# Performance work log

Measured on AMD Instinct MI355X. Metric: run time of the kernel, lower is better.

The kernel has to match this reference:

```python
import jax, jax.numpy as jnp
import numpy as np
from jax import lax

B, C, OUT, H, W = 8, 512, 512, 64, 64
BN_EPS = 1e-5


def setup_inputs() -> dict:
    key = jax.random.key(0)
    ks = jax.random.split(key, 20)
    s = 1.0 / np.sqrt(C)
    d = {
        "input1": jax.random.normal(ks[0], (B, C, H, W), jnp.float32),
        "input2": jax.random.normal(ks[1], (B, C, H, W), jnp.float32),
        "wq1": jax.random.normal(ks[2], (C, C), jnp.float32) * s,
        "bq1": jnp.zeros((C,), jnp.float32),
        "wk1": jax.random.normal(ks[3], (C, C), jnp.float32) * s,
        "bk1": jnp.zeros((C,), jnp.float32),
        "wv1": jax.random.normal(ks[4], (C, C), jnp.float32) * s,
        "bv1": jnp.zeros((C,), jnp.float32),
        "wq2": jax.random.normal(ks[5], (C, C), jnp.float32) * s,
        "bq2": jnp.zeros((C,), jnp.float32),
        "wk2": jax.random.normal(ks[6], (C, C), jnp.float32) * s,
        "bk2": jnp.zeros((C,), jnp.float32),
        "wv2": jax.random.normal(ks[7], (C, C), jnp.float32) * s,
        "bv2": jnp.zeros((C,), jnp.float32),
        "w_lin": jax.random.normal(ks[8], (1, C), jnp.float32) * s,  # shared gate conv, no bias
        "w_cat": jax.random.normal(ks[9], (OUT, 2 * C, 3, 3), jnp.float32) * (1.0 / np.sqrt(2 * C * 9)),
        "bn_gamma": jnp.ones((OUT,), jnp.float32),
        "bn_beta": jnp.zeros((OUT,), jnp.float32),
    }
    return d


def _conv1x1(x, w, b):
    # x: [B,C,H,W], w: [O,C] -> [B,O,H,W]
    return jnp.einsum('bchw,oc->bohw', x, w) + b[None, :, None, None]


def _branch(x_q_src, x_kv_src, wq, bq, wk, bk, wv, bv, w_lin, x_resid):
    # matches: attn = softmax(k(x_kv) @ q(x_q)^T); out = attn^T @ v(x_kv)
    b, c, h, w = x_kv_src.shape
    n = h * w
    q = _conv1x1(x_q_src, wq, bq).reshape(b, c, n)      # [B,C,N] (from the OTHER input)
    k = _conv1x1(x_kv_src, wk, bk).reshape(b, c, n)
    v = _conv1x1(x_kv_src, wv, bv).reshape(b, c, n)
    attn = jnp.einsum('bkn,bcn->bkc', k, q)             # [B,C,C]
    attn = jax.nn.softmax(attn, axis=-1)
    out = jnp.einsum('bkc,bkn->bcn', attn, v).reshape(b, c, h, w)
    # sigmoid gate: linear(avgpool(x_resid)) -> scalar per batch
    pooled = jnp.mean(x_resid, axis=(2, 3))             # [B,C]
    a = jax.nn.sigmoid(pooled @ w_lin.T)                # [B,1]
    return out * a[:, :, None, None] + x_resid


def reference(input1, input2, wq1, bq1, wk1, bk1, wv1, bv1,
              wq2, bq2, wk2, bk2, wv2, bv2, w_lin, w_cat, bn_gamma, bn_beta):
    # branch 1: k1 from input1, q2 from input2, v1 from input1, gate from input1
    out1 = _branch(input2, input1, wq2, bq2, wk1, bk1, wv1, bv1, w_lin, input1)
    # branch 2: k2 from input2, q1 from input1, v2 from input2, gate from input2
    out2 = _branch(input1, input2, wq1, bq1, wk2, bk2, wv2, bv2, w_lin, input2)
    x = jnp.concatenate([out1, out2], axis=1)           # [B,2C,H,W]
    y = lax.conv_general_dilated(x, w_cat, (1, 1), 'SAME',
                                 dimension_numbers=('NCHW', 'OIHW', 'NCHW'))
    # BatchNorm2d in training mode: batch statistics over (N,H,W)
    mean = jnp.mean(y, axis=(0, 2, 3), keepdims=True)
    var = jnp.var(y, axis=(0, 2, 3), keepdims=True)
    y = (y - mean) * lax.rsqrt(var + BN_EPS)
    y = y * bn_gamma[None, :, None, None] + bn_beta[None, :, None, None]
    return jax.nn.relu(y)
```

## Files before the change

### kernel.cpp

```cpp
#include <hip/hip_runtime.h>


typedef unsigned short u16;
typedef unsigned int u32;
typedef float f32x4 __attribute__((ext_vector_type(4)));
typedef short bf16x8 __attribute__((ext_vector_type(8)));

#define DEV __device__ __forceinline__

DEV u16 f2bf(float f) {
  u32 u = __float_as_uint(f);
  return (u16)((u + 0x7fffu + ((u >> 16) & 1u)) >> 16);
}
DEV float bf2f(u16 u) { return __uint_as_float(((u32)u) << 16); }

DEV void gload_lds16(const void* g, void* l) {
  __builtin_amdgcn_global_load_lds(
      (const __attribute__((address_space(1))) void*)g,
      (__attribute__((address_space(3))) void*)l, 16, 0, 0);
}

DEV void stage_tile(u16* L, const u16* src, int row0, long ld, int k0, int wid, int lane) {
  int rr = lane >> 2;
  int cc = (lane & 3) << 3;
#pragma unroll
  for (int j = 0; j < 2; ++j) {
    int chunk = j * 4 + wid;
    const u16* g = src + (long)(row0 + chunk * 16 + rr) * ld + (k0 + cc);
    gload_lds16(g, L + chunk * 512);
  }
}

DEV float waveRedSum(float v) {
#pragma unroll
  for (int o = 32; o > 0; o >>= 1) v += __shfl_xor(v, o);
  return v;
}

DEV float blockReduceSum256(float v) {
  __shared__ float r[4];
  v = waveRedSum(v);
  int tid = threadIdx.x;
  if ((tid & 63) == 0) r[tid >> 6] = v;
  __syncthreads();
  return r[0] + r[1] + r[2] + r[3];
}

__global__ __launch_bounds__(256) void gemm_gramK(const float* __restrict__ X1,
                                                  const float* __restrict__ X2,
                                                  float* __restrict__ parts)
{
  __shared__ __align__(16) u16 lds[4 * 4096];
  const int bid = blockIdx.x;
  const int cid = ((bid & 7) << 5) + (bid >> 3);
  const int z = cid >> 4, xy = cid & 15;
  const int half = z >> 3, b = z & 7;
  const int m0 = (xy & 3) * 128, n0 = (xy >> 2) * 128;
  const int tid = threadIdx.x, wid = tid >> 6, lane = tid & 63;
  const int wr = wid >> 1, wc = wid & 1;
  const int r16 = lane & 15, koff = (lane >> 4) << 3;
  const float* A = X1 + (long)b * 2097152 + half * 2048;
  const float* Bp = X2 + (long)b * 2097152 + half * 2048;
  const int sr = tid >> 3;
  const int sc = (tid & 7) * 4;

  f32x4 acc[4][4];
#pragma unroll
  for (int i = 0; i < 4; ++i)
#pragma unroll
    for (int j = 0; j < 4; ++j) acc[i][j] = (f32x4){0.f, 0.f, 0.f, 0.f};

  for (int k0 = 0; k0 < 2048; k0 += 32) {
    __syncthreads();
#pragma unroll
    for (int rr = 0; rr < 128; rr += 32) {
      float4 va = *(const float4*)&A[(long)(m0 + rr + sr) * 4096 + k0 + sc];
      float4 vb = *(const float4*)&Bp[(long)(n0 + rr + sr) * 4096 + k0 + sc];
      float fa[4] = {va.x, va.y, va.z, va.w};
      float fb[4] = {vb.x, vb.y, vb.z, vb.w};
      u32 pah0 = 0, pah1 = 0, pal0 = 0, pal1 = 0;
      u32 pbh0 = 0, pbh1 = 0, pbl0 = 0, pbl1 = 0;
#pragma unroll
      for (int e = 0; e < 2; ++e) {
        u16 h = f2bf(fa[e]);      pah0 |= ((u32)h) << (16 * e);
        u16 lo = f2bf(fa[e] - bf2f(h)); pal0 |= ((u32)lo) << (16 * e);
        h = f2bf(fa[e + 2]);      pah1 |= ((u32)h) << (16 * e);
        lo = f2bf(fa[e + 2] - bf2f(h)); pal1 |= ((u32)lo) << (16 * e);
        h = f2bf(fb[e]);          pbh0 |= ((u32)h) << (16 * e);
        lo = f2bf(fb[e] - bf2f(h)); pbl0 |= ((u32)lo) << (16 * e);
        h = f2bf(fb[e + 2]);      pbh1 |= ((u32)h) << (16 * e);
        lo = f2bf(fb[e + 2] - bf2f(h)); pbl1 |= ((u32)lo) << (16 * e);
      }
      int off = (rr + sr) * 32 + sc;
      *(uint2*)&lds[off]         = make_uint2(pah0, pah1);
      *(uint2*)&lds[4096 + off]  = make_uint2(pal0, pal1);
      *(uint2*)&lds[8192 + off]  = make_uint2(pbh0, pbh1);
      *(uint2*)&lds[12288 + off] = make_uint2(pbl0, pbl1);
    }
    __syncthreads();
    bf16x8 ah[4], al[4], bh[4], bl[4];
#pragma unroll
    for (int mi = 0; mi < 4; ++mi) {
      ah[mi] = *(const bf16x8*)&lds[(wr * 64 + mi * 16 + r16) * 32 + koff];
      al[mi] = *(const bf16x8*)&lds[4096 + (wr * 64 + mi * 16 + r16) * 32 + koff];
    }
#pragma unroll
    for (int nj = 0; nj < 4; ++nj) {
      bh[nj] = *(const bf16x8*)&lds[8192 + (wc * 64 + nj * 16 + r16) * 32 + koff];
      bl[nj] = *(const bf16x8*)&lds[12288 + (wc * 64 + nj * 16 + r16) * 32 + koff];
    }
#pragma unroll
    for (int mi = 0; mi < 4; ++mi)
#pragma unroll
      for (int nj = 0; nj < 4; ++nj) {
        acc[mi][nj] = __builtin_amdgcn_mfma_f32_16x16x32_bf16(ah[mi], bh[nj], acc[mi][nj], 0, 0, 0);
        acc[mi][nj] = __builtin_amdgcn_mfma_f32_16x16x32_bf16(ah[mi], bl[nj], acc[mi][nj], 0, 0, 0);
        acc[mi][nj] = __builtin_amdgcn_mfma_f32_16x16x32_bf16(al[mi], bh[nj], acc[mi][nj], 0, 0, 0);
      }
  }

  const int rq = lane >> 4;
  float* O = parts + (long)z * 262144;
#pragma unroll
  for (int mi = 0; mi < 4; ++mi)
#pragma unroll
    for (int nj = 0; nj < 4; ++nj)
#pragma unroll
      for (int i = 0; i < 4; ++i) {
        int row = m0 + wr * 64 + mi * 16 + rq * 4 + i;
        int col = n0 + wc * 64 + nj * 16 + r16;
        O[(long)row * 512 + col] = acc[mi][nj][i];
      }
}

__global__ __launch_bounds__(256) void k_gsplit(const float* __restrict__ parts,
                                                u16* __restrict__ Gh, u16* __restrict__ Gl)
{
  for (long i = (long)blockIdx.x * 256 + threadIdx.x; i < 2097152; i += (long)gridDim.x * 256) {
    float v = parts[i] + parts[i + 2097152];
    u16 h = f2bf(v);
    Gh[i] = h;
    Gl[i] = f2bf(v - bf2f(h));
  }
}

constexpr int EP_SPLIT = 0, EP_LOGITS = 1, EP_BF16 = 2, EP_XCAT = 3;

struct GArgs {
  const u16* Ah[2]; const u16* Al[2];
  const u16* Bh[2]; const u16* Bl[2];
  long Az[2], Bz[2];
  void* O0[2]; void* O1[2];
  const float* f0[2]; const float* f1[2];
  const float* f2[2]; const float* f3[2];
  const u16* rptr[2];
};

template <int EP, bool SPLIT3, bool FLAT>
__global__ __launch_bounds__(256) void gemm_tn2(GArgs ga, int lda, int ldb, int K, long Oz)
{
  __shared__ __align__(16) u16 lds[(SPLIT3 ? 4 : 2) * 4096];
  int bx, by, z;
  if constexpr (FLAT) {
    const int cid = ((blockIdx.x & 7) << 8) + (blockIdx.x >> 3);
    z = cid >> 7;
    const int xy = cid & 127;
    bx = xy >> 2; by = xy & 3;
  } else {
    bx = blockIdx.x; by = blockIdx.y; z = blockIdx.z;
  }
  const int br = z >> 3, b = z & 7;
  const u16* pAh = ga.Ah[br] + (long)b * ga.Az[br];
  const u16* pBh = ga.Bh[br] + (long)b * ga.Bz[br];
  const u16* pAl = SPLIT3 ? ga.Al[br] + (long)b * ga.Az[br] : nullptr;
  const u16* pBl = SPLIT3 ? ga.Bl[br] + (long)b * ga.Bz[br] : nullptr;
  const int m0 = bx * 128, n0 = by * 128;
  const int tid = threadIdx.x, wid = tid >> 6, lane = tid & 63;
  const int wr = wid >> 1, wc = wid & 1;
  const int r16 = lane & 15, koff = (lane >> 4) << 3;

  f32x4 acc[4][4];
#pragma unroll
  for (int i = 0; i < 4; ++i)
#pragma unroll
    for (int j = 0; j < 4; ++j) acc[i][j] = (f32x4){0.f, 0.f, 0.f, 0.f};

  for (int k0 = 0; k0 < K; k0 += 32) {
    __syncthreads();
    stage_tile(lds, pAh, m0, lda, k0, wid, lane);
    stage_tile(lds + 4096, pBh, n0, ldb, k0, wid, lane);
    if constexpr (SPLIT3) {
      stage_tile(lds + 8192, pAl, m0, lda, k0, wid, lane);
      stage_tile(lds + 12288, pBl, n0, ldb, k0, wid, lane);
    }
    __syncthreads();
    bf16x8 af[4], bfh[4], af2[4], bf2_[4];
#pragma unroll
    for (int mi = 0; mi < 4; ++mi)
      af[mi] = *(const bf16x8*)&lds[(wr * 64 + mi * 16 + r16) * 32 + koff];
#pragma unroll
    for (int nj = 0; nj < 4; ++nj)
      bfh[nj] = *(const bf16x8*)&lds[4096 + (wc * 64 + nj * 16 + r16) * 32 + koff];
    if constexpr (SPLIT3) {
#pragma unroll
      for (int mi = 0; mi < 4; ++mi)
        af2[mi] = *(const bf16x8*)&lds[8192 + (wr * 64 + mi * 16 + r16) * 32 + koff];
#pragma unroll
      for (int nj = 0; nj < 4; ++nj)
        bf2_[nj] = *(const bf16x8*)&lds[12288 + (wc * 64 + nj * 16 + r16) * 32 + koff];
    }
#pragma unroll
    for (int mi = 0; mi < 4; ++mi)
#pragma unroll
      for (int nj = 0; nj < 4; ++nj) {
        acc[mi][nj] = __builtin_amdgcn_mfma_f32_16x16x32_bf16(af[mi], bfh[nj], acc[mi][nj], 0, 0, 0);
        if constexpr (SPLIT3) {
          acc[mi][nj] = __builtin_amdgcn_mfma_f32_16x16x32_bf16(af[mi], bf2_[nj], acc[mi][nj], 0, 0, 0);
          acc[mi][nj] = __builtin_amdgcn_mfma_f32_16x16x32_bf16(af2[mi], bfh[nj], acc[mi][nj], 0, 0, 0);
        }
      }
  }

  const int rq = lane >> 4;
  const long off = (long)z * Oz;
  float g = 0.f;
  if constexpr (EP == EP_XCAT) g = ga.f1[br][b];
#pragma unroll
  for (int mi = 0; mi < 4; ++mi)
#pragma unroll
    for (int nj = 0; nj < 4; ++nj)
#pragma unroll
      for (int i = 0; i < 4; ++i) {
        int row = m0 + wr * 64 + mi * 16 + rq * 4 + i;
        int col = n0 + wc * 64 + nj * 16 + r16;
        float v = acc[mi][nj][i];
        if constexpr (EP == EP_SPLIT) {
          long idx = off + (long)row * 512 + col;
          u16 h = f2bf(v);
          ((u16*)ga.O0[br])[idx] = h;
          ((u16*)ga.O1[br])[idx] = f2bf(v - bf2f(h));
        } else if constexpr (EP == EP_LOGITS) {
          v += ga.f0[br][row] * ga.f3[br][b * 512 + col] + ga.f1[br][col] * ga.f2[br][b * 512 + row];
          ((float*)ga.O0[br])[off + (long)row * 512 + col] = v;
        } else if constexpr (EP == EP_BF16) {
          ((u16*)ga.O0[br])[off + (long)row * 512 + col] = f2bf(v);
        } else {
          float val = (v + ga.f0[br][b * 512 + col]) * g +
                      bf2f(ga.rptr[br][(long)b * 2097152 + (long)row * 512 + col]);
          int yy = row >> 6, xx = row & 63;
          long oidx = ((long)(b * 66 + yy + 1) * 66 + (xx + 1)) * 512 + col;
          ((u16*)ga.O0[br])[oidx] = f2bf(val);
        }
      }
}

#define MF(a, b, c) __builtin_amdgcn_mfma_f32_16x16x32_bf16(a, b, c, 0, 0, 0)
#define SCHEDB() __builtin_amdgcn_sched_barrier(0)
#define BAR() __builtin_amdgcn_s_barrier()
#define STG_B(QB, i) gload_lds16(xb + sbo[i] + kko, &lds[(QB) + ldsB0 + (i) * 4096])
#define STG_A(QB, i) gload_lds16(Arow + (i) * 294912L + Aoff, &lds[(QB) + ldsA0 + (i) * 2048])

#define PH(j, S0, S1, VMA, VMB)                                                      \
  if (pf) { S0; S1; asm volatile("s_waitcnt vmcnt(" VMA ")" ::: "memory"); }         \
  else    { asm volatile("s_waitcnt vmcnt(" VMB ")" ::: "memory"); }                 \
  BAR(); SCHEDB();                                                                   \
  {                                                                                  \
    bf16x8 a00 = *(const bf16x8*)&lds[pBase + aRd + (2 * (j)) * 1024 + sxa0];        \
    bf16x8 a01 = *(const bf16x8*)&lds[pBase + aRd + (2 * (j)) * 1024 + sxa1];        \
    bf16x8 a10 = *(const bf16x8*)&lds[pBase + aRd + (2 * (j) + 1) * 1024 + sxa0];    \
    bf16x8 a11 = *(const bf16x8*)&lds[pBase + aRd + (2 * (j) + 1) * 1024 + sxa1];    \
    asm volatile("s_waitcnt lgkmcnt(0)" ::: "memory");                               \
    SCHEDB();                                                                        \
    __builtin_amdgcn_s_setprio(1);                                                   \
    _Pragma("unroll")                                                                \
    for (int fn = 0; fn < 4; ++fn) {                                                 \
      acc[2 * (j)][fn] = MF(a00, bq[fn][0], acc[2 * (j)][fn]);                       \
      acc[2 * (j)][fn] = MF(a01, bq[fn][1], acc[2 * (j)][fn]);                       \
      acc[2 * (j) + 1][fn] = MF(a10, bq[fn][0], acc[2 * (j) + 1][fn]);               \
      acc[2 * (j) + 1][fn] = MF(a11, bq[fn][1], acc[2 * (j) + 1][fn]);               \
    }                                                                                \
    __builtin_amdgcn_s_setprio(0);                                                   \
    SCHEDB(); BAR();                                                                 \
  }

__global__ __launch_bounds__(512, 2) void k_conv8(const u16* __restrict__ W,
                                                  const u16* __restrict__ xA,
                                                  const u16* __restrict__ xB,
                                                  float* __restrict__ y,
                                                  float* __restrict__ bnsum,
                                                  float* __restrict__ bnsum2)
{
  __shared__ __align__(16) u16 lds[65536];
  const int cid = ((blockIdx.x & 7) << 5) + (blockIdx.x >> 3);
  const int bz = cid >> 5, mx = (cid >> 4) & 1, ny = cid & 15;
  const int m0 = mx * 256, n0 = ny * 256;
  const long zoff = (long)bz * 2230272;

  const int tid = threadIdx.x;
  const int w = tid >> 6, l = tid & 63;
  const int wr = w >> 2, wcn = w & 3, wl = w & 3;
  const int lr = l >> 3, l7 = l & 7, l15 = l & 15, l4 = l >> 4;
  const int ss8 = (l7 ^ lr) << 3;

  long sbo[4];
#pragma unroll
  for (int i = 0; i < 4; ++i) {
    int n = n0 + i * 64 + w * 8 + lr;
    sbo[i] = (long)((n >> 6) * 66 + (n & 63)) * 512;
  }
  const u16* Arow = W + (long)(m0 + wr * 128 + wl * 8 + lr) * 9216 + ss8;
  const int ldsA0 = wr * 8192 + wl * 512;
  const int ldsB0 = 16384 + w * 512;
  const int sxa0 = (l4 ^ l7) << 3;
  const int sxa1 = ((l4 | 4) ^ l7) << 3;
  const int aRd = wr * 8192 + l15 * 64;
  const int bRd = 16384 + wcn * 4096 + l15 * 64;

  f32x4 acc[8][4];
#pragma unroll
  for (int i = 0; i < 8; ++i)
#pragma unroll
    for (int j = 0; j < 4; ++j) acc[i][j] = (f32x4){0.f, 0.f, 0.f, 0.f};

  {
    const u16* xb = xA + zoff;
    const long kko = ss8;
    const long Aoff = 0;
    STG_B(0, 0); STG_B(0, 1); STG_B(0, 2); STG_B(0, 3);
    STG_A(0, 0); STG_A(0, 1); STG_A(0, 2); STG_A(0, 3);
  }

  for (int t = 0; t < 144; ++t) {
    const int pBase = (t & 1) << 15;
    const int qBase = pBase ^ 32768;
    const int tau = t + 1;
    const bool pf = tau < 144;
    const int ccc = tau / 9;
    const int tap = tau - ccc * 9;
    const int cch = ccc << 6;
    const u16* xb = ((cch & 512) ? xB : xA) + zoff;
    const long kko = (long)((tap / 3) * 66 + (tap % 3)) * 512 + (cch & 511) + ss8;
    const long Aoff = (long)(tap << 10) + cch;
    bf16x8 bq[4][2];

    if (pf) { STG_B(qBase, 0); STG_B(qBase, 1); asm volatile("s_waitcnt vmcnt(5)" ::: "memory"); }
    else    { asm volatile("s_waitcnt vmcnt(3)" ::: "memory"); }
    BAR(); SCHEDB();
#pragma unroll
    for (int fn = 0; fn < 4; ++fn) {
      bq[fn][0] = *(const bf16x8*)&lds[pBase + bRd + fn * 1024 + sxa0];
      bq[fn][1] = *(const bf16x8*)&lds[pBase + bRd + fn * 1024 + sxa1];
    }
    {
      bf16x8 a00 = *(const bf16x8*)&lds[pBase + aRd + 0 * 1024 + sxa0];
      bf16x8 a01 = *(const bf16x8*)&lds[pBase + aRd + 0 * 1024 + sxa1];
      bf16x8 a10 = *(const bf16x8*)&lds[pBase + aRd + 1 * 1024 + sxa0];
      bf16x8 a11 = *(const bf16x8*)&lds[pBase + aRd + 1 * 1024 + sxa1];
      asm volatile("s_waitcnt lgkmcnt(0)" ::: "memory");
      SCHEDB();
      __builtin_amdgcn_s_setprio(1);
#pragma unroll
      for (int fn = 0; fn < 4; ++fn) {
        acc[0][fn] = MF(a00, bq[fn][0], acc[0][fn]);
        acc[0][fn] = MF(a01, bq[fn][1], acc[0][fn]);
        acc[1][fn] = MF(a10, bq[fn][0], acc[1][fn]);
        acc[1][fn] = MF(a11, bq[fn][1], acc[1][fn]);
      }
      __builtin_amdgcn_s_setprio(0);
      SCHEDB(); BAR();
    }
    PH(1, STG_B(qBase, 2), STG_B(qBase, 3), "6", "2")
    PH(2, STG_A(qBase, 0), STG_A(qBase, 1), "7", "1")
    PH(3, STG_A(qBase, 2), STG_A(qBase, 3), "8", "0")
  }

#pragma unroll
  for (int fm = 0; fm < 8; ++fm)
#pragma unroll
    for (int fn = 0; fn < 4; ++fn)
#pragma unroll
      for (int i = 0; i < 4; ++i) {
        int row = m0 + wr * 128 + fm * 16 + l4 * 4 + i;
        int col = n0 + wcn * 64 + fn * 16 + l15;
        y[((long)bz * 512 + row) * 4096 + col] = acc[fm][fn][i];
      }

  __syncthreads();
  float* fl = (float*)lds;
#pragma unroll
  for (int fm = 0; fm < 8; ++fm)
#pragma unroll
    for (int i = 0; i < 4; ++i) {
      float s = acc[fm][0][i] + acc[fm][1][i] + acc[fm][2][i] + acc[fm][3][i];
      float s2 = acc[fm][0][i] * acc[fm][0][i] + acc[fm][1][i] * acc[fm][1][i] +
                 acc[fm][2][i] * acc[fm][2][i] + acc[fm][3][i] * acc[fm][3][i];
#pragma unroll
      for (int m = 1; m < 16; m <<= 1) { s += __shfl_xor(s, m); s2 += __shfl_xor(s2, m); }
      if (l15 == 0) {
        int r = wr * 128 + fm * 16 + l4 * 4 + i;
        fl[r * 4 + wcn] = s;
        fl[1024 + r * 4 + wcn] = s2;
      }
    }
  __syncthreads();
  {
    int r = tid & 255;
    int which = tid >> 8;
    const float* p = fl + which * 1024 + r * 4;
    float v = p[0] + p[1] + p[2] + p[3];
    atomicAdd((which ? bnsum2 : bnsum) + m0 + r, v);
  }
}

__global__ __launch_bounds__(256) void k_border(u16* __restrict__ xcat, float* __restrict__ rsum,
                                                float* __restrict__ bnsum)
{
  const long base = (long)blockIdx.x * 2230272;
  const int tid = threadIdx.x;
  const uint4 z4 = make_uint4(0, 0, 0, 0);
  for (int i = tid; i < 8448; i += 256) {
    long off = (i < 4224) ? (long)i * 8 : (long)65 * 66 * 512 + (long)(i - 4224) * 8;
    *(uint4*)&xcat[base + off] = z4;
  }
  for (int i = tid; i < 8192; i += 256) {
    int y = 1 + (i >> 7);
    int xsel = (i >> 6) & 1;
    int v = i & 63;
    long off = ((long)y * 66 + (xsel ? 65 : 0)) * 512 + (long)v * 8;
    *(uint4*)&xcat[base + off] = z4;
  }
  float4 f4 = {0.f, 0.f, 0.f, 0.f};
  if (blockIdx.x == 0) {
    for (int i = tid; i < 2048; i += 256) ((float4*)rsum)[i] = f4;
  } else if (blockIdx.x == 1) {
    for (int i = tid; i < 256; i += 256) ((float4*)bnsum)[i] = f4;
  }
}

__global__ __launch_bounds__(256) void k_prep(const float* __restrict__ src,
                                              u16* __restrict__ xT, float* __restrict__ rsum)
{
  __shared__ float t[64][65];
  const int b = blockIdx.z, cb = blockIdx.y, nb = blockIdx.x;
  const float* s = src + (long)b * 2097152;
  const int tid = threadIdx.x;
#pragma unroll
  for (int it = 0; it < 4; ++it) {
    int cr = it * 16 + (tid >> 4);
    int nc = (tid & 15) * 4;
    float4 v = *(const float4*)&s[(long)(cb * 64 + cr) * 4096 + nb * 64 + nc];
    t[cr][nc] = v.x; t[cr][nc + 1] = v.y; t[cr][nc + 2] = v.z; t[cr][nc + 3] = v.w;
  }
  __syncthreads();
  int nr = tid >> 2, cs = (tid & 3) * 16;
  u16 hh[16] __attribute__((aligned(16)));
#pragma unroll
  for (int j = 0; j < 16; ++j) hh[j] = f2bf(t[cs + j][nr]);
  long d = (long)b * 2097152 + (long)(nb * 64 + nr) * 512 + cb * 64 + cs;
  *(uint4*)&xT[d] = *(const uint4*)&hh[0];
  *(uint4*)&xT[d + 8] = *(const uint4*)&hh[8];
  if (tid < 64) {
    float sum = 0.f;
#pragma unroll 8
    for (int j = 0; j < 64; ++j) sum += t[tid][j];
    atomicAdd(&rsum[b * 512 + cb * 64 + tid], sum);
  }
}

__global__ __launch_bounds__(256) void k_tr(const float* __restrict__ src, u16* __restrict__ dst,
                                            int scols, int srows, long zsrc, long zdst)
{
  __shared__ float t[64][65];
  src += (long)blockIdx.z * zsrc;
  dst += (long)blockIdx.z * zdst;
  const int c0 = blockIdx.x * 64, r0 = blockIdx.y * 64;
  const int tid = threadIdx.x;
#pragma unroll
  for (int it = 0; it < 4; ++it) {
    int rr = it * 16 + (tid >> 4);
    int cc = (tid & 15) * 4;
    float4 v = *(const float4*)&src[(long)(r0 + rr) * scols + c0 + cc];
    t[rr][cc] = v.x; t[rr][cc + 1] = v.y; t[rr][cc + 2] = v.z; t[rr][cc + 3] = v.w;
  }
  __syncthreads();
  int nr = tid >> 2, cs = (tid & 3) * 16;
  u16 hh[16] __attribute__((aligned(16)));
#pragma unroll
  for (int j = 0; j < 16; ++j) hh[j] = f2bf(t[cs + j][nr]);
  long d = (long)(c0 + nr) * srows + r0 + cs;
  *(uint4*)&dst[d] = *(const uint4*)&hh[0];
  *(uint4*)&dst[d + 8] = *(const uint4*)&hh[8];
}

__global__ __launch_bounds__(256) void k_gate(const float* __restrict__ rowsum,
                                              const float* __restrict__ wlin,
                                              float* __restrict__ gates)
{
  int id = blockIdx.x;
  int inp = id >> 3, b = id & 7;
  int tid = threadIdx.x;
  float s = 0.f;
  for (int c = tid; c < 512; c += 256) s += rowsum[inp * 4096 + b * 512 + c] * wlin[c];
  s = blockReduceSum256(s);
  if (tid == 0) gates[id] = 1.f / (1.f + __expf(-s / 4096.f));
}

__global__ __launch_bounds__(256) void k_skq(const float* __restrict__ wk1, const float* __restrict__ wq2,
                                             const float* __restrict__ wk2, const float* __restrict__ wq1,
                                             const float* __restrict__ bq2, const float* __restrict__ bq1,
                                             const float* __restrict__ rowsum, float* __restrict__ S)
{
  int which = blockIdx.y, b = blockIdx.z;
  int row = blockIdx.x * 4 + (threadIdx.x >> 6);
  int lane = threadIdx.x & 63;
  const float* W; const float* rs; const float* bias = nullptr;
  if (which == 0)      { W = wk1; rs = rowsum + b * 512; }
  else if (which == 1) { W = wq2; rs = rowsum + 4096 + b * 512; bias = bq2; }
  else if (which == 2) { W = wk2; rs = rowsum + 4096 + b * 512; }
  else                 { W = wq1; rs = rowsum + b * 512; bias = bq1; }
  float s = 0.f;
  for (int i = lane; i < 512; i += 64) s += W[row * 512 + i] * rs[i];
  s = waveRedSum(s);
  if (lane == 0) S[(which * 8 + b) * 512 + row] = s + (bias ? 4096.f * bias[row] : 0.f);
}

__global__ __launch_bounds__(256) void k_mbias(const u16* __restrict__ attnT,
                                               const float* __restrict__ bv1,
                                               const float* __restrict__ bv2,
                                               float* __restrict__ mb)
{
  int z = blockIdx.y;
  int c = blockIdx.x * 4 + (threadIdx.x >> 6);
  int lane = threadIdx.x & 63;
  const float* bv = (z >= 8) ? bv2 : bv1;
  const u16* row = attnT + (long)z * 262144 + (long)c * 512;
  float s = 0.f;
  for (int k = lane; k < 512; k += 64) s += bf2f(row[k]) * bv[k];
  s = waveRedSum(s);
  if (lane == 0) mb[z * 512 + c] = s;
}

struct SplitArgs { const float* s[4]; u16* h[4]; u16* l[4]; };
__global__ __launch_bounds__(256) void k_split4(SplitArgs a)
{
  int which = blockIdx.x >> 8;
  const float* s = a.s[which];
  u16* h = a.h[which];
  u16* l = a.l[which];
  for (int i = (blockIdx.x & 255) * 256 + threadIdx.x; i < 262144; i += 65536) {
    float v = s[i];
    u16 hh = f2bf(v);
    h[i] = hh;
    l[i] = f2bf(v - bf2f(hh));
  }
}
__global__ void k_wcat(const float* __restrict__ src, u16* __restrict__ dst) {
  const int n = 512 * 9 * 1024;
  for (int i = blockIdx.x * blockDim.x + threadIdx.x; i < n; i += gridDim.x * blockDim.x) {
    int ic = i & 1023;
    int r = i >> 10;
    int t = r % 9;
    int o = r / 9;
    dst[i] = f2bf(src[((long)o * 1024 + ic) * 9 + t]);
  }
}

__global__ __launch_bounds__(256) void k_softmaxT(const float* __restrict__ L,
                                                  u16* __restrict__ attnT)
{
  const int bid = blockIdx.x;
  const int z = bid >> 4, rg = bid & 15;
  const int w = threadIdx.x >> 6, lane = threadIdx.x & 63;
  const int a0 = rg * 32 + w * 8;
  const float* Lz = L + (long)z * 262144;
  u16* Az = attnT + (long)z * 262144;
  u32 pk[8][4] = {};
#pragma unroll
  for (int it = 0; it < 8; ++it) {
    long base = (long)(a0 + it) * 512 + lane * 8;
    float4 p0 = *(const float4*)&Lz[base], p1 = *(const float4*)&Lz[base + 4];
    float v[8] = {p0.x, p0.y, p0.z, p0.w, p1.x, p1.y, p1.z, p1.w};
    float m = v[0];
#pragma unroll
    for (int j = 1; j < 8; ++j) m = fmaxf(m, v[j]);
#pragma unroll
    for (int o = 32; o > 0; o >>= 1) m = fmaxf(m, __shfl_xor(m, o));
    float e[8], s = 0.f;
#pragma unroll
    for (int j = 0; j < 8; ++j) { e[j] = __expf(v[j] - m); s += e[j]; }
    s = waveRedSum(s);
    float inv = 1.f / s;
#pragma unroll
    for (int j = 0; j < 8; ++j)
      pk[j][it >> 1] |= ((u32)f2bf(e[j] * inv)) << ((it & 1) * 16);
  }
#pragma unroll
  for (int j = 0; j < 8; ++j) {
    int c = lane * 8 + j;
    *(uint4*)&Az[(long)c * 512 + a0] = make_uint4(pk[j][0], pk[j][1], pk[j][2], pk[j][3]);
  }
}

__global__ __launch_bounds__(512) void k_bnstat(const float* __restrict__ bnsum,
                                                const float* __restrict__ bnsum2,
                                                const float* __restrict__ gamma,
                                                const float* __restrict__ beta,
                                                float* __restrict__ sc, float* __restrict__ sh)
{
  int o = threadIdx.x;
  float mean = bnsum[o] / 32768.f;
  float var = bnsum2[o] / 32768.f - mean * mean;
  float rstd = rsqrtf(var + 1e-5f);
  float scale = gamma[o] * rstd;
  sc[o] = scale;
  sh[o] = beta[o] - mean * scale;
}

__global__ __launch_bounds__(256) void k_bnapply(float* __restrict__ y,
                                                 const float* __restrict__ sc,
                                                 const float* __restrict__ sh)
{
  const long n = 16777216;
  for (long i = ((long)blockIdx.x * 256 + threadIdx.x) * 4; i < n; i += (long)gridDim.x * 1024) {
    float4 v = *(const float4*)&y[i];
    int o = (int)((i >> 12) & 511);
    float a = sc[o], c = sh[o];
    v.x = fmaxf(v.x * a + c, 0.f);
    v.y = fmaxf(v.y * a + c, 0.f);
    v.z = fmaxf(v.z * a + c, 0.f);
    v.w = fmaxf(v.w * a + c, 0.f);
    *(float4*)&y[i] = v;
  }
}

extern "C" void kernel_launch(void* const* d_in, const int* in_sizes, int n_in,
                              void* d_out, int out_size, void* d_ws, size_t ws_size,
                              hipStream_t stream)
{
  (void)in_sizes; (void)n_in; (void)out_size; (void)ws_size;
  const float* in1 = (const float*)d_in[0];
  const float* in2 = (const float*)d_in[1];
  const float* wq1 = (const float*)d_in[2];  const float* bq1 = (const float*)d_in[3];
  const float* wk1 = (const float*)d_in[4];  const float* bk1 = (const float*)d_in[5];
  const float* wv1 = (const float*)d_in[6];  const float* bv1 = (const float*)d_in[7];
  const float* wq2 = (const float*)d_in[8];  const float* bq2 = (const float*)d_in[9];
  const float* wk2 = (const float*)d_in[10]; const float* bk2 = (const float*)d_in[11];
  const float* wv2 = (const float*)d_in[12]; const float* bv2 = (const float*)d_in[13];
  const float* wlin  = (const float*)d_in[14];
  const float* wcat  = (const float*)d_in[15];
  const float* gamma = (const float*)d_in[16];
  const float* beta  = (const float*)d_in[17];

  char* ws = (char*)d_ws;
  const size_t MB = 1024ull * 1024ull;
  u16* Gh     = (u16*)(ws + 0 * MB);
  u16* Gl     = (u16*)(ws + 4 * MB);
  u16* Mb     = (u16*)(ws + 0 * MB);
  u16* Uh     = (u16*)(ws + 8 * MB);
  u16* attnT  = (u16*)(ws + 8 * MB);
  u16* Ul     = (u16*)(ws + 16 * MB);
  float* logits = (float*)(ws + 24 * MB);
  float* parts  = logits;
  u16* xcatA  = (u16*)(ws + 40 * MB);
  u16* xcatB  = xcatA + 8L * 2230272;
  u16* wcp    = (u16*)(ws + 112 * MB);
  u16* wsp    = (u16*)(ws + 122 * MB);
  u16* WvT1   = (u16*)(ws + 126 * MB);
  u16* WvT2   = WvT1 + 262144;
  float* rowsum = (float*)(ws + 127 * MB);
  float* gates  = (float*)(ws + 127 * MB + 32 * 1024);
  float* S      = (float*)(ws + 127 * MB + 36 * 1024);
  float* mb     = (float*)(ws + 127 * MB + 100 * 1024);
  float* bnsum  = (float*)(ws + 127 * MB + 132 * 1024);
  float* bnsum2 = (float*)(ws + 127 * MB + 134 * 1024);
  float* bnsc   = (float*)(ws + 127 * MB + 136 * 1024);
  float* bnsh   = (float*)(ws + 127 * MB + 138 * 1024);

  u16* wq1h = wsp + 0 * 262144; u16* wq1l = wsp + 1 * 262144;
  u16* wq2h = wsp + 2 * 262144; u16* wq2l = wsp + 3 * 262144;
  u16* wk1h = wsp + 4 * 262144; u16* wk1l = wsp + 5 * 262144;
  u16* wk2h = wsp + 6 * 262144; u16* wk2l = wsp + 7 * 262144;

  u16* xT1 = (u16*)d_out;
  u16* xT2 = (u16*)d_out + 16777216;
  float* ybuf = (float*)d_out;

  k_border<<<16, 256, 0, stream>>>(xcatA, rowsum, bnsum);
  k_prep<<<dim3(64, 8, 8), 256, 0, stream>>>(in1, xT1, rowsum);
  k_prep<<<dim3(64, 8, 8), 256, 0, stream>>>(in2, xT2, rowsum + 4096);
  k_tr<<<dim3(8, 8, 1), 256, 0, stream>>>(wv1, WvT1, 512, 512, 0L, 0L);
  k_tr<<<dim3(8, 8, 1), 256, 0, stream>>>(wv2, WvT2, 512, 512, 0L, 0L);
  {
    SplitArgs sa;
    sa.s[0] = wq1; sa.h[0] = wq1h; sa.l[0] = wq1l;
    sa.s[1] = wq2; sa.h[1] = wq2h; sa.l[1] = wq2l;
    sa.s[2] = wk1; sa.h[2] = wk1h; sa.l[2] = wk1l;
    sa.s[3] = wk2; sa.h[3] = wk2h; sa.l[3] = wk2l;
    k_split4<<<1024, 256, 0, stream>>>(sa);
  }
  k_wcat<<<4096, 256, 0, stream>>>(wcat, wcp);
  k_gate<<<16, 256, 0, stream>>>(rowsum, wlin, gates);
  k_skq<<<dim3(128, 4, 8), 256, 0, stream>>>(wk1, wq2, wk2, wq1, bq2, bq1, rowsum, S);

  gemm_gramK<<<256, 256, 0, stream>>>(in1, in2, parts);
  k_gsplit<<<2048, 256, 0, stream>>>(parts, Gh, Gl);

  {
    GArgs ga = {};
    ga.Ah[0] = wq2h; ga.Al[0] = wq2l; ga.Ah[1] = wk2h; ga.Al[1] = wk2l;
    ga.Az[0] = 0; ga.Az[1] = 0;
    ga.Bh[0] = Gh; ga.Bl[0] = Gl; ga.Bh[1] = Gh; ga.Bl[1] = Gl;
    ga.Bz[0] = 262144; ga.Bz[1] = 262144;
    ga.O0[0] = Uh; ga.O0[1] = Uh; ga.O1[0] = Ul; ga.O1[1] = Ul;
    gemm_tn2<EP_SPLIT, true, false><<<dim3(4, 4, 16), 256, 0, stream>>>(ga, 512, 512, 512, 262144);
  }
  {
    GArgs ga = {};
    ga.Ah[0] = wk1h; ga.Al[0] = wk1l; ga.Az[0] = 0;
    ga.Ah[1] = Uh + 2097152; ga.Al[1] = Ul + 2097152; ga.Az[1] = 262144;
    ga.Bh[0] = Uh; ga.Bl[0] = Ul; ga.Bz[0] = 262144;
    ga.Bh[1] = wq1h; ga.Bl[1] = wq1l; ga.Bz[1] = 0;
    ga.O0[0] = logits; ga.O0[1] = logits;
    ga.f0[0] = bk1; ga.f1[0] = bq2; ga.f2[0] = S;        ga.f3[0] = S + 4096;
    ga.f0[1] = bk2; ga.f1[1] = bq1; ga.f2[1] = S + 8192; ga.f3[1] = S + 12288;
    gemm_tn2<EP_LOGITS, true, false><<<dim3(4, 4, 16), 256, 0, stream>>>(ga, 512, 512, 512, 262144);
  }
  k_softmaxT<<<256, 256, 0, stream>>>(logits, attnT);
  k_mbias<<<dim3(128, 16), 256, 0, stream>>>(attnT, bv1, bv2, mb);
  {
    GArgs ga = {};
    ga.Ah[0] = attnT; ga.Ah[1] = attnT + 2097152;
    ga.Az[0] = 262144; ga.Az[1] = 262144;
    ga.Bh[0] = WvT1; ga.Bh[1] = WvT2; ga.Bz[0] = 0; ga.Bz[1] = 0;
    ga.O0[0] = Mb; ga.O0[1] = Mb;
    gemm_tn2<EP_BF16, false, false><<<dim3(4, 4, 16), 256, 0, stream>>>(ga, 512, 512, 512, 262144);
  }
  {
    GArgs ga = {};
    ga.Ah[0] = xT1; ga.Ah[1] = xT2; ga.Az[0] = 2097152; ga.Az[1] = 2097152;
    ga.Bh[0] = Mb; ga.Bh[1] = Mb + 2097152; ga.Bz[0] = 262144; ga.Bz[1] = 262144;
    ga.O0[0] = xcatA; ga.O0[1] = xcatB;
    ga.f0[0] = mb; ga.f0[1] = mb + 4096;
    ga.f1[0] = gates; ga.f1[1] = gates + 8;
    ga.rptr[0] = xT1; ga.rptr[1] = xT2;
    gemm_tn2<EP_XCAT, false, true><<<2048, 256, 0, stream>>>(ga, 512, 512, 512, 0);
  }

  k_conv8<<<256, 512, 0, stream>>>(wcp, xcatA, xcatB, ybuf, bnsum, bnsum2);
  k_bnstat<<<1, 512, 0, stream>>>(bnsum, bnsum2, gamma, beta, bnsc, bnsh);
  k_bnapply<<<4096, 256, 0, stream>>>(ybuf, bnsc, bnsh);
}
```

Baseline: 675.9 us.

## Split gram GEMM 4-way over K, restage conv A-reads, tile wcat transpose

The Gram GEMM now splits K into quarters instead of halves and launches twice as many blocks, to fill more CUs. The partial buffer is moved to a larger workspace region, and the reduction kernel now sums four partials. The conv kernel's inner phase schedule is reworked to double-buffer A-fragment LDS reads across phases, with adjusted vmcnt waits, so LDS latency overlaps the MFMAs. The weight-reorder kernel now transposes one output channel per block through LDS with coalesced float4 loads, in place of strided gathers. The extra partials add memory traffic in exchange for more parallelism.

New measurement: 613.6 us. -9.2%, faster.

```diff
diff --git a/kernel.cpp b/kernel.cpp
--- a/kernel.cpp
+++ b/kernel.cpp
@@ -52,15 +52,15 @@
 {
   __shared__ __align__(16) u16 lds[4 * 4096];
   const int bid = blockIdx.x;
-  const int cid = ((bid & 7) << 5) + (bid >> 3);
+  const int cid = ((bid & 7) << 6) + (bid >> 3);
   const int z = cid >> 4, xy = cid & 15;
-  const int half = z >> 3, b = z & 7;
+  const int quarter = z >> 3, b = z & 7;
   const int m0 = (xy & 3) * 128, n0 = (xy >> 2) * 128;
   const int tid = threadIdx.x, wid = tid >> 6, lane = tid & 63;
   const int wr = wid >> 1, wc = wid & 1;
   const int r16 = lane & 15, koff = (lane >> 4) << 3;
-  const float* A = X1 + (long)b * 2097152 + half * 2048;
-  const float* Bp = X2 + (long)b * 2097152 + half * 2048;
+  const float* A = X1 + (long)b * 2097152 + quarter * 1024;
+  const float* Bp = X2 + (long)b * 2097152 + quarter * 1024;
   const int sr = tid >> 3;
   const int sc = (tid & 7) * 4;
 
@@ -70,7 +70,7 @@
 #pragma unroll
     for (int j = 0; j < 4; ++j) acc[i][j] = (f32x4){0.f, 0.f, 0.f, 0.f};
 
-  for (int k0 = 0; k0 < 2048; k0 += 32) {
+  for (int k0 = 0; k0 < 1024; k0 += 32) {
     __syncthreads();
 #pragma unroll
     for (int rr = 0; rr < 128; rr += 32) {
@@ -137,7 +137,7 @@
                                                 u16* __restrict__ Gh, u16* __restrict__ Gl)
 {
   for (long i = (long)blockIdx.x * 256 + threadIdx.x; i < 2097152; i += (long)gridDim.x * 256) {
-    float v = parts[i] + parts[i + 2097152];
+    float v = parts[i] + parts[i + 2097152] + parts[i + 4194304] + parts[i + 6291456];
     u16 h = f2bf(v);
     Gh[i] = h;
     Gl[i] = f2bf(v - bf2f(h));
@@ -260,28 +260,23 @@
 #define STG_B(QB, i) gload_lds16(xb + sbo[i] + kko, &lds[(QB) + ldsB0 + (i) * 4096])
 #define STG_A(QB, i) gload_lds16(Arow + (i) * 294912L + Aoff, &lds[(QB) + ldsA0 + (i) * 2048])
 
-#define PH(j, S0, S1, VMA, VMB)                                                      \
-  if (pf) { S0; S1; asm volatile("s_waitcnt vmcnt(" VMA ")" ::: "memory"); }         \
-  else    { asm volatile("s_waitcnt vmcnt(" VMB ")" ::: "memory"); }                 \
-  BAR(); SCHEDB();                                                                   \
-  {                                                                                  \
-    bf16x8 a00 = *(const bf16x8*)&lds[pBase + aRd + (2 * (j)) * 1024 + sxa0];        \
-    bf16x8 a01 = *(const bf16x8*)&lds[pBase + aRd + (2 * (j)) * 1024 + sxa1];        \
-    bf16x8 a10 = *(const bf16x8*)&lds[pBase + aRd + (2 * (j) + 1) * 1024 + sxa0];    \
-    bf16x8 a11 = *(const bf16x8*)&lds[pBase + aRd + (2 * (j) + 1) * 1024 + sxa1];    \
-    asm volatile("s_waitcnt lgkmcnt(0)" ::: "memory");                               \
-    SCHEDB();                                                                        \
-    __builtin_amdgcn_s_setprio(1);                                                   \
-    _Pragma("unroll")                                                                \
-    for (int fn = 0; fn < 4; ++fn) {                                                 \
-      acc[2 * (j)][fn] = MF(a00, bq[fn][0], acc[2 * (j)][fn]);                       \
-      acc[2 * (j)][fn] = MF(a01, bq[fn][1], acc[2 * (j)][fn]);                       \
-      acc[2 * (j) + 1][fn] = MF(a10, bq[fn][0], acc[2 * (j) + 1][fn]);               \
-      acc[2 * (j) + 1][fn] = MF(a11, bq[fn][1], acc[2 * (j) + 1][fn]);               \
-    }                                                                                \
-    __builtin_amdgcn_s_setprio(0);                                                   \
-    SCHEDB(); BAR();                                                                 \
-  }
+#define RD_A(d, fmb)                                                        \
+  d##0 = *(const bf16x8*)&lds[pBase + aRd + (fmb) * 1024 + sxa0];           \
+  d##1 = *(const bf16x8*)&lds[pBase + aRd + (fmb) * 1024 + sxa1];           \
+  d##2 = *(const bf16x8*)&lds[pBase + aRd + ((fmb) + 1) * 1024 + sxa0];     \
+  d##3 = *(const bf16x8*)&lds[pBase + aRd + ((fmb) + 1) * 1024 + sxa1];
+
+#define MM(jj, r)                                                           \
+  __builtin_amdgcn_s_setprio(1);                                            \
+  _Pragma("unroll")                                                         \
+  for (int fn = 0; fn < 4; ++fn) {                                          \
+    acc[2 * (jj)][fn] = MF(r##0, bq[fn][0], acc[2 * (jj)][fn]);             \
+    acc[2 * (jj)][fn] = MF(r##1, bq[fn][1], acc[2 * (jj)][fn]);             \
+    acc[2 * (jj) + 1][fn] = MF(r##2, bq[fn][0], acc[2 * (jj) + 1][fn]);     \
+    acc[2 * (jj) + 1][fn] = MF(r##3, bq[fn][1], acc[2 * (jj) + 1][fn]);     \
+  }                                                                         \
+  __builtin_amdgcn_s_setprio(0);                                            \
+  SCHEDB();
 
 __global__ __launch_bounds__(512, 2) void k_conv8(const u16* __restrict__ W,
                                                   const u16* __restrict__ xA,
@@ -342,36 +337,35 @@
     const long kko = (long)((tap / 3) * 66 + (tap % 3)) * 512 + (cch & 511) + ss8;
     const long Aoff = (long)(tap << 10) + cch;
     bf16x8 bq[4][2];
-
-    if (pf) { STG_B(qBase, 0); STG_B(qBase, 1); asm volatile("s_waitcnt vmcnt(5)" ::: "memory"); }
-    else    { asm volatile("s_waitcnt vmcnt(3)" ::: "memory"); }
+    bf16x8 cA0, cA1, cA2, cA3, nA0, nA1, nA2, nA3;
+
+    if (pf) { STG_B(qBase, 0); STG_B(qBase, 1); asm volatile("s_waitcnt vmcnt(4)" ::: "memory"); }
+    else    { asm volatile("s_waitcnt vmcnt(2)" ::: "memory"); }
     BAR(); SCHEDB();
 #pragma unroll
     for (int fn = 0; fn < 4; ++fn) {
       bq[fn][0] = *(const bf16x8*)&lds[pBase + bRd + fn * 1024 + sxa0];
       bq[fn][1] = *(const bf16x8*)&lds[pBase + bRd + fn * 1024 + sxa1];
     }
-    {
-      bf16x8 a00 = *(const bf16x8*)&lds[pBase + aRd + 0 * 1024 + sxa0];
-      bf16x8 a01 = *(const bf16x8*)&lds[pBase + aRd + 0 * 1024 + sxa1];
-      bf16x8 a10 = *(const bf16x8*)&lds[pBase + aRd + 1 * 1024 + sxa0];
-      bf16x8 a11 = *(const bf16x8*)&lds[pBase + aRd + 1 * 1024 + sxa1];
-      asm volatile("s_waitcnt lgkmcnt(0)" ::: "memory");
-      SCHEDB();
-      __builtin_amdgcn_s_setprio(1);
-#pragma unroll
-      for (int fn = 0; fn < 4; ++fn) {
-        acc[0][fn] = MF(a00, bq[fn][0], acc[0][fn]);
-        acc[0][fn] = MF(a01, bq[fn][1], acc[0][fn]);
-        acc[1][fn] = MF(a10, bq[fn][0], acc[1][fn]);
-        acc[1][fn] = MF(a11, bq[fn][1], acc[1][fn]);
-      }
-      __builtin_amdgcn_s_setprio(0);
-      SCHEDB(); BAR();
-    }
-    PH(1, STG_B(qBase, 2), STG_B(qBase, 3), "6", "2")
-    PH(2, STG_A(qBase, 0), STG_A(qBase, 1), "7", "1")
-    PH(3, STG_A(qBase, 2), STG_A(qBase, 3), "8", "0")
+    RD_A(cA, 0)
+    RD_A(nA, 2)
+    SCHEDB();
+    MM(0, cA)
+    if (pf) { STG_B(qBase, 2); STG_B(qBase, 3); asm volatile("s_waitcnt vmcnt(5)" ::: "memory"); }
+    else    { asm volatile("s_waitcnt vmcnt(1)" ::: "memory"); }
+    BAR(); SCHEDB();
+    RD_A(cA, 4)
+    SCHEDB();
+    MM(1, nA)
+    if (pf) { STG_A(qBase, 0); STG_A(qBase, 1); asm volatile("s_waitcnt vmcnt(6)" ::: "memory"); }
+    else    { asm volatile("s_waitcnt vmcnt(0)" ::: "memory"); }
+    BAR(); SCHEDB();
+    RD_A(nA, 6)
+    SCHEDB();
+    MM(2, cA)
+    if (pf) { STG_A(qBase, 2); STG_A(qBase, 3); }
+    BAR(); SCHEDB();
+    MM(3, nA)
   }
 
 #pragma unroll
@@ -554,15 +548,34 @@
     l[i] = f2bf(v - bf2f(hh));
   }
 }
-__global__ void k_wcat(const float* __restrict__ src, u16* __restrict__ dst) {
-  const int n = 512 * 9 * 1024;
-  for (int i = blockIdx.x * blockDim.x + threadIdx.x; i < n; i += gridDim.x * blockDim.x) {
-    int ic = i & 1023;
-    int r = i >> 10;
-    int t = r % 9;
-    int o = r / 9;
-    dst[i] = f2bf(src[((long)o * 1024 + ic) * 9 + t]);
-  }
+
+__global__ __launch_bounds__(256) void k_wcat(const float* __restrict__ src, u16* __restrict__ dst)
+{
+  __shared__ float t[9 * 1029];
+  const int o = blockIdx.x;
+  const int tid = threadIdx.x;
+  const float* s = src + (long)o * 9216;
+#pragma unroll
+  for (int it = 0; it < 9; ++it) {
+    int f4 = it * 256 + tid;
+    float4 v = *(const float4*)&s[f4 * 4];
+    float va[4] = {v.x, v.y, v.z, v.w};
+    int f = f4 * 4;
+#pragma unroll
+    for (int e = 0; e < 4; ++e) {
+      int ic = (f + e) / 9, tp = (f + e) - ic * 9;
+      t[tp * 1029 + ic] = va[e];
+    }
+  }
+  __syncthreads();
+  u16* d = dst + (long)o * 9216;
+#pragma unroll
+  for (int tp = 0; tp < 9; ++tp)
+#pragma unroll
+    for (int c = 0; c < 4; ++c) {
+      int ic = c * 256 + tid;
+      d[tp * 1024 + ic] = f2bf(t[tp * 1029 + ic]);
+    }
 }
 
 __global__ __launch_bounds__(256) void k_softmaxT(const float* __restrict__ L,
@@ -660,7 +673,7 @@
   u16* attnT  = (u16*)(ws + 8 * MB);
   u16* Ul     = (u16*)(ws + 16 * MB);
   float* logits = (float*)(ws + 24 * MB);
-  float* parts  = logits;
+  float* parts  = (float*)(ws + 8 * MB);
   u16* xcatA  = (u16*)(ws + 40 * MB);
   u16* xcatB  = xcatA + 8L * 2230272;
   u16* wcp    = (u16*)(ws + 112 * MB);
@@ -698,11 +711,11 @@
     sa.s[3] = wk2; sa.h[3] = wk2h; sa.l[3] = wk2l;
     k_split4<<<1024, 256, 0, stream>>>(sa);
   }
-  k_wcat<<<4096, 256, 0, stream>>>(wcat, wcp);
+  k_wcat<<<512, 256, 0, stream>>>(wcat, wcp);
   k_gate<<<16, 256, 0, stream>>>(rowsum, wlin, gates);
   k_skq<<<dim3(128, 4, 8), 256, 0, stream>>>(wk1, wq2, wk2, wq1, bq2, bq1, rowsum, S);
 
-  gemm_gramK<<<256, 256, 0, stream>>>(in1, in2, parts);
+  gemm_gramK<<<512, 256, 0, stream>>>(in1, in2, parts);
   k_gsplit<<<2048, 256, 0, stream>>>(parts, Gh, Gl);
 
   {
```
